# Kernel optimization log

Measured on AMD Instinct MI355X. Metric: run time of the kernel, lower is better.

## Reference

```python
import jax, jax.numpy as jnp
import numpy as np

H = 768; R = 16; L = 3; NS = 128; NQ = 128


def setup_inputs():
    key = jax.random.key(0)
    ks = iter(jax.random.split(key, 40))
    def w(shape, s=0.02):
        return (s * jax.random.normal(next(ks), shape)).astype(jnp.float32)
    return {
        "support_features": jax.random.normal(next(ks), (NS, H), jnp.float32),
        "support_labels": jax.random.randint(next(ks), (NS,), 0, 3),
        "query_features": jax.random.normal(next(ks), (NQ, H), jnp.float32),
        "sim_w1": w((H, 2 * H)), "sim_b1": jnp.zeros((H,), jnp.float32),
        "sim_w2": w((R, H)), "sim_b2": jnp.zeros((R,), jnp.float32),
        "div_w1": w((H, 2 * H)), "div_b1": jnp.zeros((H,), jnp.float32),
        "div_w2": w((R, H)), "div_b2": jnp.zeros((R,), jnp.float32),
        "rel_w": w((L, R, H, H)), "rel_b": jnp.zeros((L, R, H), jnp.float32),
        "agg_w1": w((L, H, 2 * H)), "agg_b1": jnp.zeros((L, H), jnp.float32),
        "agg_w2": w((L, H, H)), "agg_b2": jnp.zeros((L, H), jnp.float32),
        "ln_g": jnp.ones((L, H), jnp.float32), "ln_b": jnp.zeros((L, H), jnp.float32),
        "cls_w1": w((H // 2, H)), "cls_b1": jnp.zeros((H // 2,), jnp.float32),
        "cls_w2": w((3, H // 2)), "cls_b2": jnp.zeros((3,), jnp.float32),
    }


def _symmetrize(F):
    # torch loop fills [i,j] and [j,i] with value computed from pair (min(i,j), max(i,j)); diag stays 0
    N = F.shape[0]
    idx = jnp.arange(N)
    lower = (idx[:, None] > idx[None, :])
    Fs = jnp.where(lower[:, :, None], jnp.swapaxes(F, 0, 1), F)
    off = (idx[:, None] != idx[None, :]).astype(F.dtype)
    return Fs * off[:, :, None]


def _relations(x, w1, b1, w2, b2, diversity):
    h = x.shape[1]
    wa, wb = w1[:, :h], w1[:, h:]  # split concat([a,b]) @ w1^T into two matmuls
    pa = x @ wa.T                  # [N,H], contribution of first element (x_i)
    if diversity:
        d = jnp.abs(x[:, None, :] - x[None, :, :])   # [N,N,H]
        hid = jax.nn.relu(pa[:, None, :] + d @ wb.T + b1)
    else:
        pb = x @ wb.T
        hid = jax.nn.relu(pa[:, None, :] + pb[None, :, :] + b1)
    logits = hid @ w2.T + b2       # [N,N,R]
    return _symmetrize(jax.nn.softmax(logits, axis=-1))


def _layer_norm(y, g, b):
    mu = y.mean(-1, keepdims=True)
    var = ((y - mu) ** 2).mean(-1, keepdims=True)
    return (y - mu) / jnp.sqrt(var + 1e-5) * g + b


def _prop_layer(x, C, rw, rb, aw1, ab1, aw2, ab2, g, b):
    N = x.shape[0]
    T = jnp.einsum('jh,rkh->jrk', x, rw) + rb       # per-relation transform [N,R,H]
    msg = jnp.einsum('ijr,jrk->ik', C, T) / (N - 1)  # mean over N-1 neighbors (diag of C is 0)
    comb = jnp.concatenate([x, msg], axis=-1)
    agg = jax.nn.relu(comb @ aw1.T + ab1) @ aw2.T + ab2
    return _layer_norm(agg + x, g, b)


def reference(support_features, support_labels, query_features,
              sim_w1, sim_b1, sim_w2, sim_b2,
              div_w1, div_b1, div_w2, div_b2,
              rel_w, rel_b, agg_w1, agg_b1, agg_w2, agg_b2, ln_g, ln_b,
              cls_w1, cls_b1, cls_w2, cls_b2):
    all_x = jnp.concatenate([support_features, query_features], axis=0)
    sim = _relations(all_x, sim_w1, sim_b1, sim_w2, sim_b2, diversity=False)
    div = _relations(all_x, div_w1, div_b1, div_w2, div_b2, diversity=True)
    C = (sim + div) * 0.5
    x = all_x
    for l in range(L):
        x = _prop_layer(x, C, rel_w[l], rel_b[l], agg_w1[l], agg_b1[l],
                        agg_w2[l], agg_b2[l], ln_g[l], ln_b[l])
    q = x[support_features.shape[0]:]
    preds = jax.nn.relu(q @ cls_w1.T + cls_b1) @ cls_w2.T + cls_b2  # dropout = identity (eval)
    return preds, sim, div, x
```

## Files before the change

kernel.cpp:

```cpp
#include <hip/hip_runtime.h>
#include <hip/hip_bf16.h>


typedef __attribute__((ext_vector_type(8))) short s16x8;
typedef __attribute__((ext_vector_type(4))) float f32x4;

__device__ __forceinline__ short f2bf_s(float f){
  union { __hip_bfloat16 h; short s; } u; u.h = __float2bfloat16(f); return u.s;
}
__device__ __forceinline__ float bf_s2f(short s){
  union { __hip_bfloat16 h; short s; } u; u.s = s; return __bfloat162float(u.h);
}
__device__ __forceinline__ f32x4 mfma16(s16x8 a, s16x8 b, f32x4 c){
  return __builtin_amdgcn_mfma_f32_16x16x32_bf16(a, b, c, 0, 0, 0);
}
__device__ __forceinline__ void gload16(void* lds, const void* g){
  __builtin_amdgcn_global_load_lds((const __attribute__((address_space(1))) void*)g,
                                   (__attribute__((address_space(3))) void*)lds,
                                   16, 0, 0);
}
__device__ __forceinline__ unsigned pack2bf(float lo, float hi){
  return __builtin_amdgcn_perm(__float_as_uint(hi), __float_as_uint(lo), 0x07060302u);
}
__device__ __forceinline__ s16x8 absdiff_bf(uint4 a, uint4 b){
  union { s16x8 v; unsigned u[4]; } o;
  const unsigned au[4] = {a.x,a.y,a.z,a.w}, bu[4] = {b.x,b.y,b.z,b.w};
  #pragma unroll
  for (int w = 0; w < 4; ++w){
    float dlo = __uint_as_float(au[w] << 16)         - __uint_as_float(bu[w] << 16);
    float dhi = __uint_as_float(au[w] & 0xffff0000u) - __uint_as_float(bu[w] & 0xffff0000u);
    unsigned r;
    asm("v_cvt_pk_bf16_f32 %0, abs(%1), abs(%2)" : "=v"(r) : "v"(dlo), "v"(dhi));
    o.u[w] = r;
  }
  return o.v;
}

__device__ __forceinline__ void tri_decode(int b, int& i0, int& j0){
  int jb = (int)((sqrtf(2.f*(float)b + 1.f) - 1.f)*0.5f);
  while (2*(jb+1)*(jb+2) <= b) ++jb;
  while (2*jb*(jb+1) > b) --jb;
  i0 = (b - 2*jb*(jb+1))*4;
  j0 = jb*16;
}
__device__ __forceinline__ void tri_decode32(int b, int& i0, int& j0){
  int jb = (int)((sqrtf((float)b + 1.f) - 1.f)*0.5f);
  while (4*(jb+1)*(jb+2) <= b) ++jb;
  while (4*jb*(jb+1) > b) --jb;
  i0 = (b - 4*jb*(jb+1))*4;
  j0 = jb*32;
}

template<int BM, int BN, int EPI>
__global__ __launch_bounds__(256) void gemm_bt2(
    const short* __restrict__ A, int lda,
    const short* __restrict__ B, int ldb,
    float* __restrict__ Cf, short* __restrict__ Cb, int ldc,
    const float* __restrict__ bias, int K, int NT)
{
  __shared__ short As[BM*128];
  __shared__ short Bs[BN*128];
  const int tid = threadIdx.x, lane = tid & 63, wid = tid >> 6;
  const int nt = blockIdx.x % NT, mt = blockIdx.x / NT;
  const int m0 = mt*BM, n0 = nt*BN;
  const int wm0 = (wid>>1)*(BM/2), wn0 = (wid&1)*(BN/2);
  f32x4 acc[BM/32][BN/32] = {};
  for (int k0 = 0; k0 < K; k0 += 128){
    if (k0) __syncthreads();
    #pragma unroll
    for (int q = 0; q < BM/16; ++q){
      const int d = (wid*(BM/16)+q)*1024 + lane*16;
      const int row = d>>8, c = d&255;
      gload16((char*)As + (wid*(BM/16)+q)*1024,
              (const char*)A + (size_t)(m0+row)*lda*2 + (size_t)k0*2 + (c ^ ((row&7)<<4)));
    }
    #pragma unroll
    for (int q = 0; q < BN/16; ++q){
      const int d = (wid*(BN/16)+q)*1024 + lane*16;
      const int row = d>>8, c = d&255;
      gload16((char*)Bs + (wid*(BN/16)+q)*1024,
              (const char*)B + (size_t)(n0+row)*ldb*2 + (size_t)k0*2 + (c ^ ((row&7)<<4)));
    }
    __syncthreads();
    #pragma unroll
    for (int kk = 0; kk < 4; ++kk){
      const int colb = (kk*32 + (lane>>4)*8)*2;
      s16x8 af[BM/32], bfv[BN/32];
      #pragma unroll
      for (int mi = 0; mi < BM/32; ++mi){
        const int row = wm0 + mi*16 + (lane&15);
        af[mi] = *(const s16x8*)((char*)As + row*256 + (colb ^ ((row&7)<<4)));
      }
      #pragma unroll
      for (int ni = 0; ni < BN/32; ++ni){
        const int row = wn0 + ni*16 + (lane&15);
        bfv[ni] = *(const s16x8*)((char*)Bs + row*256 + (colb ^ ((row&7)<<4)));
      }
      #pragma unroll
      for (int mi = 0; mi < BM/32; ++mi)
        #pragma unroll
        for (int ni = 0; ni < BN/32; ++ni)
          acc[mi][ni] = mfma16(af[mi], bfv[ni], acc[mi][ni]);
    }
  }
  #pragma unroll
  for (int mi = 0; mi < BM/32; ++mi){
    #pragma unroll
    for (int ni = 0; ni < BN/32; ++ni){
      const int gcol = n0 + wn0 + ni*16 + (lane&15);
      const float bv = bias[gcol];
      #pragma unroll
      for (int r = 0; r < 4; ++r){
        const int grow = m0 + wm0 + mi*16 + (lane>>4)*4 + r;
        float v = acc[mi][ni][r] + bv;
        if (EPI == 2) v = fmaxf(v, 0.f);
        if (EPI == 3) Cf[(size_t)grow*ldc + gcol] = v;
        else          Cb[(size_t)grow*ldc + gcol] = f2bf_s(v);
      }
    }
  }
}

__global__ __launch_bounds__(256) void gemm_msg(
    const short* __restrict__ A,
    const short* __restrict__ B,
    float* __restrict__ slabs)
{
  __shared__ short As[64*64];
  __shared__ short Bs[64*64];
  const int tid = threadIdx.x, lane = tid & 63, wid = tid >> 6;
  const int mt = blockIdx.x / 12, nt = blockIdx.x % 12;
  const int m0 = mt*64, n0 = nt*64, kc0 = blockIdx.y*512;
  const int wm0 = (wid>>1)*32, wn0 = (wid&1)*32;
  f32x4 acc[2][2] = {};
  for (int s = 0; s < 8; ++s){
    const int k0 = kc0 + s*64;
    if (s) __syncthreads();
    #pragma unroll
    for (int q = 0; q < 2; ++q){
      const int d = (wid*2+q)*1024 + lane*16;
      const int row = d>>7, c = d&127;
      gload16((char*)As + (wid*2+q)*1024,
              (const char*)A + (size_t)(m0+row)*8192 + (size_t)k0*2 + (c ^ ((row&7)<<4)));
    }
    #pragma unroll
    for (int rd = 0; rd < 2; ++rd){
      int ei = rd*2048 + tid*8, kr = ei>>6, nc = ei&63;
      union { uint4 v; short s4[8]; } u;
      u.v = *(const uint4*)(B + (size_t)(k0+kr)*768 + n0 + nc);
      #pragma unroll
      for (int e = 0; e < 8; ++e)
        *(short*)((char*)Bs + (nc+e)*128 + ((kr*2) ^ (((nc+e)&7)<<4))) = u.s4[e];
    }
    __syncthreads();
    #pragma unroll
    for (int kk = 0; kk < 2; ++kk){
      const int colb = (kk*32 + (lane>>4)*8)*2;
      s16x8 af[2], bfv[2];
      #pragma unroll
      for (int mi = 0; mi < 2; ++mi){
        const int row = wm0 + mi*16 + (lane&15);
        af[mi] = *(const s16x8*)((char*)As + row*128 + (colb ^ ((row&7)<<4)));
      }
      #pragma unroll
      for (int ni = 0; ni < 2; ++ni){
        const int row = wn0 + ni*16 + (lane&15);
        bfv[ni] = *(const s16x8*)((char*)Bs + row*128 + (colb ^ ((row&7)<<4)));
      }
      #pragma unroll
      for (int mi = 0; mi < 2; ++mi)
        #pragma unroll
        for (int ni = 0; ni < 2; ++ni)
          acc[mi][ni] = mfma16(af[mi], bfv[ni], acc[mi][ni]);
    }
  }
  float* out = slabs + (size_t)blockIdx.y*196608;
  #pragma unroll
  for (int mi = 0; mi < 2; ++mi)
    #pragma unroll
    for (int ni = 0; ni < 2; ++ni){
      const int gcol = n0 + wn0 + ni*16 + (lane&15);
      #pragma unroll
      for (int r = 0; r < 4; ++r){
        const int grow = m0 + wm0 + mi*16 + (lane>>4)*4 + r;
        out[(size_t)grow*768 + gcol] = acc[mi][ni][r];
      }
    }
}

__global__ void msgsum(const float* __restrict__ slabs, short* __restrict__ comb){
  const int i = (blockIdx.x*256 + threadIdx.x)*4;
  if (i >= 196608) return;
  float4 s = {0.f,0.f,0.f,0.f};
  #pragma unroll
  for (int c = 0; c < 8; ++c){
    float4 v = *(const float4*)(slabs + (size_t)c*196608 + i);
    s.x += v.x; s.y += v.y; s.z += v.z; s.w += v.w;
  }
  const float sc = 1.f/255.f;
  const int row = i/768, col = i%768;
  union { uint2 u; short s4[4]; } o;
  o.s4[0]=f2bf_s(s.x*sc); o.s4[1]=f2bf_s(s.y*sc);
  o.s4[2]=f2bf_s(s.z*sc); o.s4[3]=f2bf_s(s.w*sc);
  *(uint2*)(comb + (size_t)row*1536 + 768 + col) = o.u;
}

__global__ __launch_bounds__(512, 4) void pairrel4(
    const short* __restrict__ xb,
    const short* __restrict__ wbdiv,
    const float* __restrict__ P2,
    const short* __restrict__ w2d_g,
    float* __restrict__ Ldp)
{
  __shared__ short Bs[2*256*64];
  const int tid = threadIdx.x, lane = tid & 63, wv = tid >> 6;
  const int ip = wv >> 2, jj = (wv >> 1) & 1, wc = wv & 1;
  int i0, j0; tri_decode32(blockIdx.x, i0, j0);
  const int nt = blockIdx.y, n0 = nt*256;

  const short* xjp  = xb + (size_t)(j0 + jj*16 + (lane&15))*1536 + (lane>>4)*8;
  const short* xi0p = xb + (size_t)(i0 + 2*ip    )*1536 + (lane>>4)*8;
  const short* xi1p = xb + (size_t)(i0 + 2*ip + 1)*1536 + (lane>>4)*8;

  #pragma unroll
  for (int q = 0; q < 4; ++q){
    const int d = (wv*4+q)*1024 + lane*16;
    const int row = d>>7, c = d&127;
    gload16((char*)Bs + (wv*4+q)*1024,
            (const char*)wbdiv + (size_t)(n0+row)*1536 + (c ^ ((row&7)<<4)));
  }

  f32x4 acc[2][8] = {};
  for (int t = 0; t < 12; ++t){
    uint4 uja  = *(const uint4*)(xjp  + t*64);
    uint4 ujb  = *(const uint4*)(xjp  + t*64 + 32);
    uint4 ui0a = *(const uint4*)(xi0p + t*64);
    uint4 ui0b = *(const uint4*)(xi0p + t*64 + 32);
    uint4 ui1a = *(const uint4*)(xi1p + t*64);
    uint4 ui1b = *(const uint4*)(xi1p + t*64 + 32);
    if (t < 11){
      char* dst = (char*)Bs + ((t+1)&1)*32768;
      const char* src = (const char*)wbdiv + (size_t)(t+1)*128;
      #pragma unroll
      for (int q = 0; q < 4; ++q){
        const int d = (wv*4+q)*1024 + lane*16;
        const int row = d>>7, c = d&127;
        gload16(dst + (wv*4+q)*1024, src + (size_t)(n0+row)*1536 + (c ^ ((row&7)<<4)));
      }
    }
    __builtin_amdgcn_sched_barrier(0);
    if (t < 11) asm volatile("s_waitcnt vmcnt(10)" ::: "memory");
    else        asm volatile("s_waitcnt vmcnt(6)"  ::: "memory");
    __builtin_amdgcn_s_barrier();
    __builtin_amdgcn_sched_barrier(0);
    const char* bufc = (const char*)Bs + (t&1)*32768;
    #pragma unroll
    for (int kk = 0; kk < 2; ++kk){
      s16x8 af0 = absdiff_bf(kk ? ujb : uja, kk ? ui0b : ui0a);
      s16x8 af1 = absdiff_bf(kk ? ujb : uja, kk ? ui1b : ui1a);
      const int colb = (kk*32 + (lane>>4)*8)*2;
      #pragma unroll
      for (int ni = 0; ni < 8; ++ni){
        const int row = wc*128 + ni*16 + (lane&15);
        s16x8 bv = *(const s16x8*)(bufc + row*128 + (colb ^ ((row&7)<<4)));
        acc[0][ni] = mfma16(af0, bv, acc[0][ni]);
        acc[1][ni] = mfma16(af1, bv, acc[1][ni]);
      }
    }
    __builtin_amdgcn_sched_barrier(0);
    __builtin_amdgcn_s_barrier();
  }
  __syncthreads();

  float* red = (float*)((char*)Bs + 32768);
  #pragma unroll
  for (int h = 0; h < 2; ++h){
    if (ip == h){
      #pragma unroll
      for (int mi = 0; mi < 2; ++mi){
        const float* pr = P2 + (size_t)(i0 + 2*h + mi)*2304 + 1536 + n0;
        #pragma unroll
        for (int ni = 0; ni < 8; ++ni){
          const int col = wc*128 + ni*16 + (lane&15);
          const float pav = pr[col];
          #pragma unroll
          for (int r = 0; r < 4; ++r){
            const int lrow = mi*32 + jj*16 + (lane>>4)*4 + r;
            const float v = fmaxf(acc[mi][ni][r] + pav, 0.f);
            *(short*)((char*)Bs + lrow*512 + ((col*2) ^ ((lrow&7)<<4))) =
                (short)(__float_as_uint(v) >> 16);
          }
        }
      }
    }
    __syncthreads();
    const int kh = wv >> 2, rq = wv & 3;
    f32x4 a2 = {0.f,0.f,0.f,0.f};
    const int arow = rq*16 + (lane&15);
    #pragma unroll
    for (int q = 0; q < 4; ++q){
      const int k = kh*128 + q*32 + (lane>>4)*8;
      s16x8 a = *(const s16x8*)((char*)Bs + arow*512 + ((k*2) ^ ((arow&7)<<4)));
      s16x8 w = *(const s16x8*)(w2d_g + (size_t)(lane&15)*768 + n0 + k);
      a2 = mfma16(a, w, a2);
    }
    if (kh == 1){
      #pragma unroll
      for (int r = 0; r < 4; ++r)
        red[(rq*16 + (lane>>4)*4 + r)*16 + (lane&15)] = a2[r];
    }
    __syncthreads();
    if (kh == 0){
      #pragma unroll
      for (int r = 0; r < 4; ++r){
        const int lrow = rq*16 + (lane>>4)*4 + r;
        const int p = h*64 + lrow;
        const int i = i0 + (p>>5), j = j0 + (p&31);
        Ldp[(size_t)nt*1048576 + (((size_t)i<<8) + j)*16 + (lane&15)]
          = a2[r] + red[lrow*16 + (lane&15)];
      }
    }
    __syncthreads();
  }
}

__global__ __launch_bounds__(256) void simpart(
    const float* __restrict__ P2,
    const short* __restrict__ w2s_g,
    float* __restrict__ Ls)
{
  __shared__ short Hs[64*256];
  const int tid = threadIdx.x, lane = tid & 63, wv = tid >> 6;
  int i0, j0; tri_decode(blockIdx.x, i0, j0);
  const int arow = wv*16 + (lane&15);
  f32x4 acc2 = {0.f,0.f,0.f,0.f};
  for (int nt = 0; nt < 3; ++nt){
    const int n0 = nt*256;
    if (nt) __syncthreads();
    {
      const int row = tid>>2, c0 = (tid&3)*64;
      const float* pap = P2 + (size_t)(i0 + (row>>4))*2304 + n0 + c0;
      const float* pbp = P2 + (size_t)(j0 + (row&15))*2304 + 768 + n0 + c0;
      #pragma unroll
      for (int cc = 0; cc < 64; cc += 8){
        float4 a0 = *(const float4*)(pap+cc), a1 = *(const float4*)(pap+cc+4);
        float4 q0 = *(const float4*)(pbp+cc), q1 = *(const float4*)(pbp+cc+4);
        uint4 o;
        o.x = pack2bf(fmaxf(a0.x+q0.x,0.f), fmaxf(a0.y+q0.y,0.f));
        o.y = pack2bf(fmaxf(a0.z+q0.z,0.f), fmaxf(a0.w+q0.w,0.f));
        o.z = pack2bf(fmaxf(a1.x+q1.x,0.f), fmaxf(a1.y+q1.y,0.f));
        o.w = pack2bf(fmaxf(a1.z+q1.z,0.f), fmaxf(a1.w+q1.w,0.f));
        *(uint4*)((char*)Hs + row*512 + (((c0+cc)*2) ^ ((row&7)<<4))) = o;
      }
    }
    __syncthreads();
    #pragma unroll
    for (int q = 0; q < 8; ++q){
      const int colb = (q*32 + (lane>>4)*8)*2;
      s16x8 a = *(const s16x8*)((const char*)Hs + arow*512 + (colb ^ ((arow&7)<<4)));
      s16x8 w = *(const s16x8*)(w2s_g + (size_t)(lane&15)*768 + n0 + q*32 + (lane>>4)*8);
      acc2 = mfma16(a, w, acc2);
    }
  }
  const int r_ = lane & 15;
  #pragma unroll
  for (int r = 0; r < 4; ++r){
    const int p = wv*16 + (lane>>4)*4 + r;
    const int i = i0 + (p>>4), j = j0 + (p&15);
    Ls[(((size_t)i<<8) + j)*16 + r_] = acc2[r];
  }
}

__global__ __launch_bounds__(256) void finisher2(
    const float* __restrict__ Ls, const float* __restrict__ Ldp,
    const float* __restrict__ b2s, const float* __restrict__ b2d,
    float* __restrict__ simo, float* __restrict__ divo, short* __restrict__ Cb)
{
  const int p = blockIdx.x*256 + threadIdx.x;
  const int i = p >> 8, j = p & 255;
  float so[16], dd[16];
  if (i == j){
    #pragma unroll
    for (int r = 0; r < 16; ++r){ so[r] = 0.f; dd[r] = 0.f; }
  } else {
    const int si = i < j ? i : j, sj = i < j ? j : i;
    const size_t base = (((size_t)si << 8) + sj) * 16;
    float mx = -1e30f, sum;
    #pragma unroll
    for (int r = 0; r < 16; ++r){ so[r] = Ls[base+r] + b2s[r]; mx = fmaxf(mx, so[r]); }
    sum = 0.f;
    #pragma unroll
    for (int r = 0; r < 16; ++r){ so[r] = expf(so[r]-mx); sum += so[r]; }
    sum = 1.f/sum;
    #pragma unroll
    for (int r = 0; r < 16; ++r) so[r] *= sum;
    mx = -1e30f;
    #pragma unroll
    for (int r = 0; r < 16; ++r){
      dd[r] = Ldp[base+r] + Ldp[base+r+1048576] + Ldp[base+r+2097152] + b2d[r];
      mx = fmaxf(mx, dd[r]);
    }
    sum = 0.f;
    #pragma unroll
    for (int r = 0; r < 16; ++r){ dd[r] = expf(dd[r]-mx); sum += dd[r]; }
    sum = 1.f/sum;
    #pragma unroll
    for (int r = 0; r < 16; ++r) dd[r] *= sum;
  }
  const size_t ob = (size_t)p * 16;
  #pragma unroll
  for (int r = 0; r < 16; ++r){
    simo[ob+r] = so[r];
    divo[ob+r] = dd[r];
    Cb[ob+r]   = f2bf_s(0.5f*(so[r]+dd[r]));
  }
}

__global__ __launch_bounds__(256) void gemm_relT(
    const short* __restrict__ A,
    const float* __restrict__ Bf,
    short* __restrict__ T,
    const float* __restrict__ bias)
{
  __shared__ short As[128*64];
  __shared__ short Bs[64*64];
  const int tid = threadIdx.x, lane = tid & 63, wv = tid >> 6;
  const int nt = blockIdx.x >> 1, mt = blockIdx.x & 1;
  const int n0 = nt*64, m0 = mt*128;
  const int wm = wv >> 1, wn = wv & 1;
  const int brow = tid >> 2, q4 = tid & 3;
  f32x4 acc[4][2] = {};
  for (int k0 = 0; k0 < 768; k0 += 64){
    if (k0) __syncthreads();
    #pragma unroll
    for (int q = 0; q < 4; ++q){
      const int d = (wv*4+q)*1024 + lane*16;
      const int row = d>>7, c = d&127;
      gload16((char*)As + (wv*4+q)*1024,
              (const char*)A + (size_t)(m0+row)*3072 + (size_t)k0*2 + (c ^ ((row&7)<<4)));
    }
    {
      const float* bp = Bf + (size_t)(n0+brow)*768 + k0 + q4*16;
      float4 v0 = *(const float4*)bp,      v1 = *(const float4*)(bp+4);
      float4 v2 = *(const float4*)(bp+8),  v3 = *(const float4*)(bp+12);
      union { uint4 v; unsigned u[4]; } ua, ub;
      ua.u[0]=pack2bf(v0.x,v0.y); ua.u[1]=pack2bf(v0.z,v0.w);
      ua.u[2]=pack2bf(v1.x,v1.y); ua.u[3]=pack2bf(v1.z,v1.w);
      ub.u[0]=pack2bf(v2.x,v2.y); ub.u[1]=pack2bf(v2.z,v2.w);
      ub.u[2]=pack2bf(v3.x,v3.y); ub.u[3]=pack2bf(v3.z,v3.w);
      const int bc = q4*32;
      *(uint4*)((char*)Bs + brow*128 + ((bc   ) ^ ((brow&7)<<4))) = ua.v;
      *(uint4*)((char*)Bs + brow*128 + ((bc+16) ^ ((brow&7)<<4))) = ub.v;
    }
    __syncthreads();
    #pragma unroll
    for (int kk = 0; kk < 2; ++kk){
      const int kb = kk*64 + (lane>>4)*16;
      s16x8 af[4], bfv[2];
      #pragma unroll
      for (int mi = 0; mi < 4; ++mi){
        const int row = wm*64 + mi*16 + (lane&15);
        af[mi] = *(const s16x8*)((char*)As + row*128 + (kb ^ ((row&7)<<4)));
      }
      #pragma unroll
      for (int ni = 0; ni < 2; ++ni){
        const int row = wn*32 + ni*16 + (lane&15);
        bfv[ni] = *(const s16x8*)((char*)Bs + row*128 + (kb ^ ((row&7)<<4)));
      }
      #pragma unroll
      for (int mi = 0; mi < 4; ++mi)
        #pragma unroll
        for (int ni = 0; ni < 2; ++ni)
          acc[mi][ni] = mfma16(af[mi], bfv[ni], acc[mi][ni]);
    }
  }
  #pragma unroll
  for (int mi = 0; mi < 4; ++mi)
    #pragma unroll
    for (int ni = 0; ni < 2; ++ni){
      const int nn = n0 + wn*32 + ni*16 + (lane&15);
      const float bv = bias[nn];
      #pragma unroll
      for (int r = 0; r < 4; ++r){
        const int row = m0 + wm*64 + mi*16 + (lane>>4)*4 + r;
        T[(size_t)row*12288 + nn] = f2bf_s(acc[mi][ni][r] + bv);
      }
    }
}

__global__ __launch_bounds__(256) void ln_kernel(
    const float* __restrict__ y, float* __restrict__ x, short* __restrict__ combx,
    const float* __restrict__ g, const float* __restrict__ b, float* __restrict__ xfinal)
{
  const int row = blockIdx.x, tid = threadIdx.x;
  float tv[3]; float s = 0.f, s2 = 0.f;
  #pragma unroll
  for (int c = 0; c < 3; ++c){
    const int idx = tid + c*256;
    const float v = y[row*768+idx] + x[row*768+idx];
    tv[c] = v; s += v; s2 += v*v;
  }
  #pragma unroll
  for (int off = 32; off > 0; off >>= 1){ s += __shfl_down(s, off); s2 += __shfl_down(s2, off); }
  __shared__ float red[8];
  const int wid = tid >> 6, lane = tid & 63;
  if (lane == 0){ red[wid] = s; red[wid+4] = s2; }
  __syncthreads();
  if (tid == 0){
    red[0] = red[0]+red[1]+red[2]+red[3];
    red[4] = red[4]+red[5]+red[6]+red[7];
  }
  __syncthreads();
  const float mu = red[0]*(1.f/768.f);
  const float var = red[4]*(1.f/768.f) - mu*mu;
  const float inv = rsqrtf(var + 1e-5f);
  #pragma unroll
  for (int c = 0; c < 3; ++c){
    const int idx = tid + c*256;
    const float v = (tv[c]-mu)*inv*g[idx] + b[idx];
    x[row*768+idx] = v;
    combx[(size_t)row*1536 + idx] = f2bf_s(v);
    if (xfinal) xfinal[row*768+idx] = v;
  }
}

__device__ __forceinline__ void cvt4(const float* __restrict__ s,
                                     short* __restrict__ d, int i, int n){
  if (i >= n) return;
  float4 v = *(const float4*)(s+i);
  union { uint2 u; short s4[4]; } o;
  o.s4[0]=f2bf_s(v.x); o.s4[1]=f2bf_s(v.y); o.s4[2]=f2bf_s(v.z); o.s4[3]=f2bf_s(v.w);
  *(uint2*)(d+i) = o.u;
}

__global__ void setup_all(
    const float* __restrict__ sim_w2, const float* __restrict__ div_w2,
    const float* __restrict__ agg_w1, const float* __restrict__ agg_w2,
    const float* __restrict__ cls_w1, const float* __restrict__ sim_w1,
    const float* __restrict__ div_w1, const float* __restrict__ sup,
    const float* __restrict__ qry, const float* __restrict__ sim_b1,
    const float* __restrict__ div_b1,
    short* __restrict__ W2S, short* __restrict__ W2D, short* __restrict__ AW1,
    short* __restrict__ AW2, short* __restrict__ CW1, short* __restrict__ W1X4,
    float* __restrict__ XF, short* __restrict__ COMB, float* __restrict__ B1C)
{
  const int b = blockIdx.x, tid = threadIdx.x;
  if (b < 12)        cvt4(sim_w2, W2S, (b*256+tid)*4, 12288);
  else if (b < 24)   cvt4(div_w2, W2D, ((b-12)*256+tid)*4, 12288);
  else if (b < 3480) cvt4(agg_w1, AW1, ((b-24)*256+tid)*4, 3538944);
  else if (b < 5208) cvt4(agg_w2, AW2, ((b-3480)*256+tid)*4, 1769472);
  else if (b < 5496) cvt4(cls_w1, CW1, ((b-5208)*256+tid)*4, 294912);
  else if (b < 7800){
    const int i = ((b-5496)*256+tid)*4;
    if (i < 2359296){
      const int mat = i / 589824, rem = i % 589824;
      const int r = rem / 768, c = rem % 768;
      const float* src = (mat < 2 ? sim_w1 : div_w1) + (size_t)r*1536 + (mat&1)*768 + c;
      float4 v = *(const float4*)src;
      union { uint2 u; short s4[4]; } o;
      o.s4[0]=f2bf_s(v.x); o.s4[1]=f2bf_s(v.y); o.s4[2]=f2bf_s(v.z); o.s4[3]=f2bf_s(v.w);
      *(uint2*)(W1X4+i) = o.u;
    }
  } else if (b < 7992){
    const int i = ((b-7800)*256+tid)*4;
    if (i < 196608){
      const int row = i / 768, col = i % 768;
      const float* s = (row < 128 ? sup + (size_t)row*768 : qry + (size_t)(row-128)*768) + col;
      float4 v = *(const float4*)s;
      *(float4*)(XF+i) = v;
      union { uint2 u; short s4[4]; } o;
      o.s4[0]=f2bf_s(v.x); o.s4[1]=f2bf_s(v.y); o.s4[2]=f2bf_s(v.z); o.s4[3]=f2bf_s(v.w);
      *(uint2*)(COMB + (size_t)row*1536 + col) = o.u;
    }
  } else {
    for (int t = tid; t < 2304; t += 256)
      B1C[t] = (t < 768) ? sim_b1[t] : ((t < 1536) ? 0.f : div_b1[t-1536]);
  }
}

__global__ void cls2_kernel(const short* __restrict__ hc, const float* __restrict__ w2,
                            const float* __restrict__ b2, float* __restrict__ preds){
  const int t = blockIdx.x*192 + threadIdx.x;
  if (t >= 384) return;
  const int m = t/3, c = t - m*3;
  float s = b2[c];
  for (int k = 0; k < 384; ++k)
    s += bf_s2f(hc[m*384+k]) * w2[c*384+k];
  preds[m*3+c] = s;
}

static const size_t OFF_B1CAT = 0;
static const size_t OFF_LS    = 16384;
static const size_t OFF_MSGF  = 4210688;
static const size_t OFF_LDP   = 10502144;
static const size_t OFF_P     = 23085056;
static const size_t OFF_XF    = 25444352;
static const size_t OFF_Y     = 26230784;
static const size_t OFF_COMB  = 27017216;
static const size_t OFF_CB    = 27803648;
static const size_t OFF_W1X4  = 29900800;
static const size_t OFF_W2S   = 34619392;
static const size_t OFF_W2D   = 34643968;
static const size_t OFF_AW1   = 34668544;
static const size_t OFF_AW2   = 41746432;
static const size_t OFF_CW1   = 45285376;
static const size_t OFF_TBUF  = 45875200;
static const size_t OFF_HID1  = 52166656;
static const size_t OFF_HIDC  = 52559872;

extern "C" void kernel_launch(void* const* d_in, const int* in_sizes, int n_in,
                              void* d_out, int out_size, void* d_ws, size_t ws_size,
                              hipStream_t stream)
{
  (void)in_sizes; (void)n_in; (void)out_size; (void)ws_size;
  const float* sup    = (const float*)d_in[0];
  const float* qry    = (const float*)d_in[2];
  const float* sim_w1 = (const float*)d_in[3];
  const float* sim_b1 = (const float*)d_in[4];
  const float* sim_w2 = (const float*)d_in[5];
  const float* sim_b2 = (const float*)d_in[6];
  const float* div_w1 = (const float*)d_in[7];
  const float* div_b1 = (const float*)d_in[8];
  const float* div_w2 = (const float*)d_in[9];
  const float* div_b2 = (const float*)d_in[10];
  const float* rel_w  = (const float*)d_in[11];
  const float* rel_b  = (const float*)d_in[12];
  const float* agg_w1 = (const float*)d_in[13];
  const float* agg_b1 = (const float*)d_in[14];
  const float* agg_w2 = (const float*)d_in[15];
  const float* agg_b2 = (const float*)d_in[16];
  const float* ln_g   = (const float*)d_in[17];
  const float* ln_b   = (const float*)d_in[18];
  const float* cls_w1 = (const float*)d_in[19];
  const float* cls_b1 = (const float*)d_in[20];
  const float* cls_w2 = (const float*)d_in[21];
  const float* cls_b2 = (const float*)d_in[22];

  char* w = (char*)d_ws;
  float* B1C  = (float*)(w + OFF_B1CAT);
  float* LS   = (float*)(w + OFF_LS);
  float* MSGF = (float*)(w + OFF_MSGF);
  float* LDP  = (float*)(w + OFF_LDP);
  float* P2   = (float*)(w + OFF_P);
  float* XF   = (float*)(w + OFF_XF);
  float* Y    = (float*)(w + OFF_Y);
  short* COMB = (short*)(w + OFF_COMB);
  short* CB   = (short*)(w + OFF_CB);
  short* W1X4 = (short*)(w + OFF_W1X4);
  short* W2S  = (short*)(w + OFF_W2S);
  short* W2D  = (short*)(w + OFF_W2D);
  short* AW1  = (short*)(w + OFF_AW1);
  short* AW2  = (short*)(w + OFF_AW2);
  short* CW1  = (short*)(w + OFF_CW1);
  short* TBUF = (short*)(w + OFF_TBUF);
  short* HID1 = (short*)(w + OFF_HID1);
  short* HIDC = (short*)(w + OFF_HIDC);

  float* preds = (float*)d_out;
  float* simo  = preds + 384;
  float* divo  = simo + 1048576;
  float* xout  = divo + 1048576;

  setup_all<<<7993, 256, 0, stream>>>(sim_w2, div_w2, agg_w1, agg_w2, cls_w1,
                                      sim_w1, div_w1, sup, qry, sim_b1, div_b1,
                                      W2S, W2D, AW1, AW2, CW1, W1X4, XF, COMB, B1C);

  gemm_bt2<64,64,3><<<144, 256, 0, stream>>>(COMB, 1536, W1X4, 768, P2, nullptr, 2304,
                                             B1C, 768, 36);

  pairrel4<<<dim3(288,3), 512, 0, stream>>>(COMB, W1X4 + (size_t)3*589824, P2, W2D, LDP);
  simpart<<<544, 256, 0, stream>>>(P2, W2S, LS);
  finisher2<<<256, 256, 0, stream>>>(LS, LDP, sim_b2, div_b2, simo, divo, CB);

  for (int l = 0; l < 3; ++l){
    gemm_relT<<<384, 256, 0, stream>>>(COMB, rel_w + (size_t)l*9437184, TBUF,
                                       rel_b + l*12288);
    gemm_msg<<<dim3(48,8), 256, 0, stream>>>(CB, TBUF, MSGF);
    msgsum<<<192, 256, 0, stream>>>(MSGF, COMB);
    gemm_bt2<32,32,2><<<192, 256, 0, stream>>>(COMB, 1536, AW1 + (size_t)l*1179648, 1536,
                                               nullptr, HID1, 768, agg_b1 + l*768, 1536, 24);
    gemm_bt2<32,32,3><<<192, 256, 0, stream>>>(HID1, 768, AW2 + (size_t)l*589824, 768,
                                               Y, nullptr, 768, agg_b2 + l*768, 768, 24);
    ln_kernel<<<256, 256, 0, stream>>>(Y, XF, COMB, ln_g + l*768, ln_b + l*768,
                                       (l == 2) ? xout : nullptr);
  }

  gemm_bt2<32,32,2><<<48, 256, 0, stream>>>(COMB + (size_t)128*1536, 1536, CW1, 768,
                                            nullptr, HIDC, 384, cls_b1, 768, 12);
  cls2_kernel<<<2, 192, 0, stream>>>(HIDC, cls_w2, cls_b2, preds);
}
```

Before: 305.3 us.

## Fuse sim-relation pass into pair kernel and use fp16 packed absdiff

The similarity logits kernel is folded into the diversity pair kernel as an extra grid slice (blockIdx.y==3) using 32x32 triangular tiles, removing one launch and letting both run concurrently. The |x_i - x_j| operand is now computed with a single packed fp16 subtract plus a sign mask instead of bf16 unpack/convert, feeding fp16 MFMAs, which requires new fp16 copies of x and the div weight built in setup. This trades bf16 range for fp16 precision and adds setup work and extra workspace.

```diff
diff --git a/kernel.cpp b/kernel.cpp
--- a/kernel.cpp
+++ b/kernel.cpp
@@ -1,5 +1,6 @@
 #include <hip/hip_runtime.h>
 #include <hip/hip_bf16.h>
+#include <hip/hip_fp16.h>
 
 
 typedef __attribute__((ext_vector_type(8))) short s16x8;
@@ -11,8 +12,14 @@
 __device__ __forceinline__ float bf_s2f(short s){
   union { __hip_bfloat16 h; short s; } u; u.s = s; return __bfloat162float(u.h);
 }
+__device__ __forceinline__ short f2h_s(float f){
+  union { __half h; short s; } u; u.h = __float2half(f); return u.s;
+}
 __device__ __forceinline__ f32x4 mfma16(s16x8 a, s16x8 b, f32x4 c){
   return __builtin_amdgcn_mfma_f32_16x16x32_bf16(a, b, c, 0, 0, 0);
+}
+__device__ __forceinline__ f32x4 mfma16h(s16x8 a, s16x8 b, f32x4 c){
+  return __builtin_amdgcn_mfma_f32_16x16x32_f16(a, b, c, 0, 0, 0);
 }
 __device__ __forceinline__ void gload16(void* lds, const void* g){
   __builtin_amdgcn_global_load_lds((const __attribute__((address_space(1))) void*)g,
@@ -22,27 +29,19 @@
 __device__ __forceinline__ unsigned pack2bf(float lo, float hi){
   return __builtin_amdgcn_perm(__float_as_uint(hi), __float_as_uint(lo), 0x07060302u);
 }
-__device__ __forceinline__ s16x8 absdiff_bf(uint4 a, uint4 b){
+__device__ __forceinline__ s16x8 absdiff_h(uint4 a, uint4 b){
   union { s16x8 v; unsigned u[4]; } o;
   const unsigned au[4] = {a.x,a.y,a.z,a.w}, bu[4] = {b.x,b.y,b.z,b.w};
   #pragma unroll
   for (int w = 0; w < 4; ++w){
-    float dlo = __uint_as_float(au[w] << 16)         - __uint_as_float(bu[w] << 16);
-    float dhi = __uint_as_float(au[w] & 0xffff0000u) - __uint_as_float(bu[w] & 0xffff0000u);
-    unsigned r;
-    asm("v_cvt_pk_bf16_f32 %0, abs(%1), abs(%2)" : "=v"(r) : "v"(dlo), "v"(dhi));
-    o.u[w] = r;
+    unsigned d;
+    asm("v_pk_add_f16 %0, %1, %2 neg_lo:[0,1] neg_hi:[0,1]"
+        : "=v"(d) : "v"(au[w]), "v"(bu[w]));
+    o.u[w] = d & 0x7fff7fffu;
   }
   return o.v;
 }
 
-__device__ __forceinline__ void tri_decode(int b, int& i0, int& j0){
-  int jb = (int)((sqrtf(2.f*(float)b + 1.f) - 1.f)*0.5f);
-  while (2*(jb+1)*(jb+2) <= b) ++jb;
-  while (2*jb*(jb+1) > b) --jb;
-  i0 = (b - 2*jb*(jb+1))*4;
-  j0 = jb*16;
-}
 __device__ __forceinline__ void tri_decode32(int b, int& i0, int& j0){
   int jb = (int)((sqrtf((float)b + 1.f) - 1.f)*0.5f);
   while (4*(jb+1)*(jb+2) <= b) ++jb;
@@ -205,29 +204,73 @@
   *(uint2*)(comb + (size_t)row*1536 + 768 + col) = o.u;
 }
 
-__global__ __launch_bounds__(512, 4) void pairrel4(
-    const short* __restrict__ xb,
-    const short* __restrict__ wbdiv,
+__global__ __launch_bounds__(512, 4) void pairrel5(
+    const short* __restrict__ xh,
+    const short* __restrict__ wbdh,
     const float* __restrict__ P2,
     const short* __restrict__ w2d_g,
-    float* __restrict__ Ldp)
+    const short* __restrict__ w2s_g,
+    float* __restrict__ Ldp,
+    float* __restrict__ Ls)
 {
   __shared__ short Bs[2*256*64];
   const int tid = threadIdx.x, lane = tid & 63, wv = tid >> 6;
+  int i0, j0; tri_decode32(blockIdx.x, i0, j0);
+
+  if (blockIdx.y == 3){
+    f32x4 acc2 = {0.f,0.f,0.f,0.f};
+    const int arow = wv*16 + (lane&15);
+    for (int nt = 0; nt < 3; ++nt){
+      const int n0 = nt*256;
+      if (nt) __syncthreads();
+      {
+        const int row = tid>>2, c0 = (tid&3)*64;
+        const float* pap = P2 + (size_t)(i0 + (row>>5))*2304 + n0 + c0;
+        const float* pbp = P2 + (size_t)(j0 + (row&31))*2304 + 768 + n0 + c0;
+        #pragma unroll
+        for (int cc = 0; cc < 64; cc += 8){
+          float4 a0 = *(const float4*)(pap+cc), a1 = *(const float4*)(pap+cc+4);
+          float4 q0 = *(const float4*)(pbp+cc), q1 = *(const float4*)(pbp+cc+4);
+          uint4 o;
+          o.x = pack2bf(fmaxf(a0.x+q0.x,0.f), fmaxf(a0.y+q0.y,0.f));
+          o.y = pack2bf(fmaxf(a0.z+q0.z,0.f), fmaxf(a0.w+q0.w,0.f));
+          o.z = pack2bf(fmaxf(a1.x+q1.x,0.f), fmaxf(a1.y+q1.y,0.f));
+          o.w = pack2bf(fmaxf(a1.z+q1.z,0.f), fmaxf(a1.w+q1.w,0.f));
+          *(uint4*)((char*)Bs + row*512 + (((c0+cc)*2) ^ ((row&7)<<4))) = o;
+        }
+      }
+      __syncthreads();
+      #pragma unroll
+      for (int q = 0; q < 8; ++q){
+        const int colb = (q*32 + (lane>>4)*8)*2;
+        s16x8 a = *(const s16x8*)((const char*)Bs + arow*512 + (colb ^ ((arow&7)<<4)));
+        s16x8 w = *(const s16x8*)(w2s_g + (size_t)(lane&15)*768 + n0 + q*32 + (lane>>4)*8);
+        acc2 = mfma16(a, w, acc2);
+      }
+    }
+    const int r_ = lane & 15;
+    #pragma unroll
+    for (int r = 0; r < 4; ++r){
+      const int p = wv*16 + (lane>>4)*4 + r;
+      const int i = i0 + (p>>5), j = j0 + (p&31);
+      Ls[(((size_t)i<<8) + j)*16 + r_] = acc2[r];
+    }
+    return;
+  }
+
   const int ip = wv >> 2, jj = (wv >> 1) & 1, wc = wv & 1;
-  int i0, j0; tri_decode32(blockIdx.x, i0, j0);
   const int nt = blockIdx.y, n0 = nt*256;
 
-  const short* xjp  = xb + (size_t)(j0 + jj*16 + (lane&15))*1536 + (lane>>4)*8;
-  const short* xi0p = xb + (size_t)(i0 + 2*ip    )*1536 + (lane>>4)*8;
-  const short* xi1p = xb + (size_t)(i0 + 2*ip + 1)*1536 + (lane>>4)*8;
+  const short* xjp  = xh + (size_t)(j0 + jj*16 + (lane&15))*768 + (lane>>4)*8;
+  const short* xi0p = xh + (size_t)(i0 + 2*ip    )*768 + (lane>>4)*8;
+  const short* xi1p = xh + (size_t)(i0 + 2*ip + 1)*768 + (lane>>4)*8;
 
   #pragma unroll
   for (int q = 0; q < 4; ++q){
     const int d = (wv*4+q)*1024 + lane*16;
     const int row = d>>7, c = d&127;
     gload16((char*)Bs + (wv*4+q)*1024,
-            (const char*)wbdiv + (size_t)(n0+row)*1536 + (c ^ ((row&7)<<4)));
+            (const char*)wbdh + (size_t)(n0+row)*1536 + (c ^ ((row&7)<<4)));
   }
 
   f32x4 acc[2][8] = {};
@@ -240,7 +283,7 @@
     uint4 ui1b = *(const uint4*)(xi1p + t*64 + 32);
     if (t < 11){
       char* dst = (char*)Bs + ((t+1)&1)*32768;
-      const char* src = (const char*)wbdiv + (size_t)(t+1)*128;
+      const char* src = (const char*)wbdh + (size_t)(t+1)*128;
       #pragma unroll
       for (int q = 0; q < 4; ++q){
         const int d = (wv*4+q)*1024 + lane*16;
@@ -256,15 +299,15 @@
     const char* bufc = (const char*)Bs + (t&1)*32768;
     #pragma unroll
     for (int kk = 0; kk < 2; ++kk){
-      s16x8 af0 = absdiff_bf(kk ? ujb : uja, kk ? ui0b : ui0a);
-      s16x8 af1 = absdiff_bf(kk ? ujb : uja, kk ? ui1b : ui1a);
+      s16x8 af0 = absdiff_h(kk ? ujb : uja, kk ? ui0b : ui0a);
+      s16x8 af1 = absdiff_h(kk ? ujb : uja, kk ? ui1b : ui1a);
       const int colb = (kk*32 + (lane>>4)*8)*2;
       #pragma unroll
       for (int ni = 0; ni < 8; ++ni){
         const int row = wc*128 + ni*16 + (lane&15);
         s16x8 bv = *(const s16x8*)(bufc + row*128 + (colb ^ ((row&7)<<4)));
-        acc[0][ni] = mfma16(af0, bv, acc[0][ni]);
-        acc[1][ni] = mfma16(af1, bv, acc[1][ni]);
+        acc[0][ni] = mfma16h(af0, bv, acc[0][ni]);
+        acc[1][ni] = mfma16h(af1, bv, acc[1][ni]);
       }
     }
     __builtin_amdgcn_sched_barrier(0);
@@ -321,53 +364,6 @@
       }
     }
     __syncthreads();
-  }
-}
-
-__global__ __launch_bounds__(256) void simpart(
-    const float* __restrict__ P2,
-    const short* __restrict__ w2s_g,
-    float* __restrict__ Ls)
-{
-  __shared__ short Hs[64*256];
-  const int tid = threadIdx.x, lane = tid & 63, wv = tid >> 6;
-  int i0, j0; tri_decode(blockIdx.x, i0, j0);
-  const int arow = wv*16 + (lane&15);
-  f32x4 acc2 = {0.f,0.f,0.f,0.f};
-  for (int nt = 0; nt < 3; ++nt){
-    const int n0 = nt*256;
-    if (nt) __syncthreads();
-    {
-      const int row = tid>>2, c0 = (tid&3)*64;
-      const float* pap = P2 + (size_t)(i0 + (row>>4))*2304 + n0 + c0;
-      const float* pbp = P2 + (size_t)(j0 + (row&15))*2304 + 768 + n0 + c0;
-      #pragma unroll
-      for (int cc = 0; cc < 64; cc += 8){
-        float4 a0 = *(const float4*)(pap+cc), a1 = *(const float4*)(pap+cc+4);
-        float4 q0 = *(const float4*)(pbp+cc), q1 = *(const float4*)(pbp+cc+4);
-        uint4 o;
-        o.x = pack2bf(fmaxf(a0.x+q0.x,0.f), fmaxf(a0.y+q0.y,0.f));
-        o.y = pack2bf(fmaxf(a0.z+q0.z,0.f), fmaxf(a0.w+q0.w,0.f));
-        o.z = pack2bf(fmaxf(a1.x+q1.x,0.f), fmaxf(a1.y+q1.y,0.f));
-        o.w = pack2bf(fmaxf(a1.z+q1.z,0.f), fmaxf(a1.w+q1.w,0.f));
-        *(uint4*)((char*)Hs + row*512 + (((c0+cc)*2) ^ ((row&7)<<4))) = o;
-      }
-    }
-    __syncthreads();
-    #pragma unroll
-    for (int q = 0; q < 8; ++q){
-      const int colb = (q*32 + (lane>>4)*8)*2;
-      s16x8 a = *(const s16x8*)((const char*)Hs + arow*512 + (colb ^ ((arow&7)<<4)));
-      s16x8 w = *(const s16x8*)(w2s_g + (size_t)(lane&15)*768 + n0 + q*32 + (lane>>4)*8);
-      acc2 = mfma16(a, w, acc2);
-    }
-  }
-  const int r_ = lane & 15;
-  #pragma unroll
-  for (int r = 0; r < 4; ++r){
-    const int p = wv*16 + (lane>>4)*4 + r;
-    const int i = i0 + (p>>4), j = j0 + (p&15);
-    Ls[(((size_t)i<<8) + j)*16 + r_] = acc2[r];
   }
 }
 
@@ -542,7 +538,8 @@
     const float* __restrict__ div_b1,
     short* __restrict__ W2S, short* __restrict__ W2D, short* __restrict__ AW1,
     short* __restrict__ AW2, short* __restrict__ CW1, short* __restrict__ W1X4,
-    float* __restrict__ XF, short* __restrict__ COMB, float* __restrict__ B1C)
+    float* __restrict__ XF, short* __restrict__ COMB, float* __restrict__ B1C,
+    short* __restrict__ XH, short* __restrict__ WBDH)
 {
   const int b = blockIdx.x, tid = threadIdx.x;
   if (b < 12)        cvt4(sim_w2, W2S, (b*256+tid)*4, 12288);
@@ -571,10 +568,22 @@
       union { uint2 u; short s4[4]; } o;
       o.s4[0]=f2bf_s(v.x); o.s4[1]=f2bf_s(v.y); o.s4[2]=f2bf_s(v.z); o.s4[3]=f2bf_s(v.w);
       *(uint2*)(COMB + (size_t)row*1536 + col) = o.u;
-    }
-  } else {
+      union { uint2 u; short s4[4]; } oh;
+      oh.s4[0]=f2h_s(v.x); oh.s4[1]=f2h_s(v.y); oh.s4[2]=f2h_s(v.z); oh.s4[3]=f2h_s(v.w);
+      *(uint2*)(XH + i) = oh.u;
+    }
+  } else if (b < 7993){
     for (int t = tid; t < 2304; t += 256)
       B1C[t] = (t < 768) ? sim_b1[t] : ((t < 1536) ? 0.f : div_b1[t-1536]);
+  } else {
+    const int i = ((b-7993)*256+tid)*4;
+    if (i < 589824){
+      const int r = i / 768, c = i % 768;
+      float4 v = *(const float4*)(div_w1 + (size_t)r*1536 + 768 + c);
+      union { uint2 u; short s4[4]; } o;
+      o.s4[0]=f2h_s(v.x); o.s4[1]=f2h_s(v.y); o.s4[2]=f2h_s(v.z); o.s4[3]=f2h_s(v.w);
+      *(uint2*)(WBDH + i) = o.u;
+    }
   }
 }
 
@@ -607,6 +616,8 @@
 static const size_t OFF_TBUF  = 45875200;
 static const size_t OFF_HID1  = 52166656;
 static const size_t OFF_HIDC  = 52559872;
+static const size_t OFF_XH    = 52658176;
+static const size_t OFF_WBDH  = 53051392;
 
 extern "C" void kernel_launch(void* const* d_in, const int* in_sizes, int n_in,
                               void* d_out, int out_size, void* d_ws, size_t ws_size,
@@ -655,21 +666,23 @@
   short* TBUF = (short*)(w + OFF_TBUF);
   short* HID1 = (short*)(w + OFF_HID1);
   short* HIDC = (short*)(w + OFF_HIDC);
+  short* XH   = (short*)(w + OFF_XH);
+  short* WBDH = (short*)(w + OFF_WBDH);
 
   float* preds = (float*)d_out;
   float* simo  = preds + 384;
   float* divo  = simo + 1048576;
   float* xout  = divo + 1048576;
 
-  setup_all<<<7993, 256, 0, stream>>>(sim_w2, div_w2, agg_w1, agg_w2, cls_w1,
+  setup_all<<<8569, 256, 0, stream>>>(sim_w2, div_w2, agg_w1, agg_w2, cls_w1,
                                       sim_w1, div_w1, sup, qry, sim_b1, div_b1,
-                                      W2S, W2D, AW1, AW2, CW1, W1X4, XF, COMB, B1C);
+                                      W2S, W2D, AW1, AW2, CW1, W1X4, XF, COMB, B1C,
+                                      XH, WBDH);
 
   gemm_bt2<64,64,3><<<144, 256, 0, stream>>>(COMB, 1536, W1X4, 768, P2, nullptr, 2304,
                                              B1C, 768, 36);
 
-  pairrel4<<<dim3(288,3), 512, 0, stream>>>(COMB, W1X4 + (size_t)3*589824, P2, W2D, LDP);
-  simpart<<<544, 256, 0, stream>>>(P2, W2S, LS);
+  pairrel5<<<dim3(288,4), 512, 0, stream>>>(XH, WBDH, P2, W2D, W2S, LDP, LS);
   finisher2<<<256, 256, 0, stream>>>(LS, LDP, sim_b2, div_b2, simo, divo, CB);
 
   for (int l = 0; l < 3; ++l){
```

After: 321.2 us. +5.2%, slower.
